# Optimization experiments

Hardware: AMD Instinct MI355X
Metric: run time of the kernel (lower is better)

## Reference

```python
import jax, jax.numpy as jnp
import numpy as np
import math

N = 60000          # nodes per node type
M = 60000          # edges per edge type
H = 64             # hidden_dim
PE = 4             # pe_dim
L = 3              # message passing layers
E = 24             # edge types
PE_LEN = 2 * N     # pe table length = 2 * num_pick_nodes
T = 6              # node types: object, ssBox, place_frame, ssCylinder, pick, place

# (src_type, dst_type) index per edge type, following detailed_edge_types order
SRC = np.array([0,1,2,1,2,0,4,5,0,1,2,3,0,4,2,4,3,4,0,5,3,5,2,5])
DST = np.array([1,0,1,2,0,2,5,4,0,1,2,3,4,0,4,2,4,3,5,0,5,3,5,2])


def posenc(n, d):
    pos = jnp.arange(n, dtype=jnp.float32)[:, None]
    div = jnp.exp(jnp.arange(0, d, 2, dtype=jnp.float32) * (-math.log(10000.0) / d))
    ang = pos * div  # [n, d//2]
    return jnp.stack([jnp.sin(ang), jnp.cos(ang)], axis=-1).reshape(n, d)


def setup_inputs():
    key = jax.random.key(0)
    ks = iter(jax.random.split(key, 48))
    def n_(shape, fan):
        return jax.random.normal(next(ks), shape, dtype=jnp.float32) / np.sqrt(fan).astype(np.float32)
    def ti(shape, hi):
        return jax.random.randint(next(ks), shape, 0, hi, dtype=jnp.int32)
    inp = {}
    inp['x_object'] = jax.random.normal(next(ks), (N, 4), dtype=jnp.float32)
    inp['x_ssBox'] = jax.random.normal(next(ks), (N, 4), dtype=jnp.float32)
    inp['x_place_frame'] = jax.random.normal(next(ks), (N, 4), dtype=jnp.float32)
    inp['x_ssCylinder'] = jax.random.normal(next(ks), (N, 3), dtype=jnp.float32)
    for nt in ['object', 'ssBox', 'place_frame', 'ssCylinder', 'pick', 'place']:
        inp['times_' + nt] = ti((N,), PE_LEN)
    inp['edge_index'] = ti((E, 2, M), N)
    inp['W_object'] = n_((8, H), 8); inp['b_object'] = jnp.zeros((H,), jnp.float32)
    inp['W_ssBox'] = n_((8, H), 8); inp['b_ssBox'] = jnp.zeros((H,), jnp.float32)
    inp['W_place_frame'] = n_((8, H), 8); inp['b_place_frame'] = jnp.zeros((H,), jnp.float32)
    inp['W_ssCylinder'] = n_((7, H), 7); inp['b_ssCylinder'] = jnp.zeros((H,), jnp.float32)
    inp['W_pick'] = n_((PE, H), PE); inp['b_pick'] = jnp.zeros((H,), jnp.float32)
    inp['W_place'] = n_((PE, H), PE); inp['b_place'] = jnp.zeros((H,), jnp.float32)
    inp['Wl'] = n_((L, E, H, H), H)
    inp['bl'] = jnp.zeros((L, E, H), jnp.float32)
    inp['Wr'] = n_((L, E, H, H), H)
    inp['Wm1'] = n_((H, H // 4), H); inp['bm1'] = jnp.zeros((H // 4,), jnp.float32)
    inp['Wm2'] = n_((H // 4, 1), H // 4); inp['bm2'] = jnp.zeros((1,), jnp.float32)
    return inp


def _forward(x_object, x_ssBox, x_place_frame, x_ssCylinder,
             W_object, b_object, W_ssBox, b_ssBox, W_place_frame, b_place_frame,
             W_ssCylinder, b_ssCylinder, W_pick, b_pick, W_place, b_place,
             Wl, bl, Wr, Wm1, bm1, Wm2, bm2,
             times_object, times_ssBox, times_place_frame, times_ssCylinder,
             times_pick, times_place, edge_index):
    pe = posenc(PE_LEN, PE)
    def emb(x, t, W, b):  # features || pe[times] -> linear
        return jnp.concatenate([x, pe[t]], axis=1) @ W + b
    X = jnp.stack([
        emb(x_object, times_object, W_object, b_object),
        emb(x_ssBox, times_ssBox, W_ssBox, b_ssBox),
        emb(x_place_frame, times_place_frame, W_place_frame, b_place_frame),
        emb(x_ssCylinder, times_ssCylinder, W_ssCylinder, b_ssCylinder),
        pe[times_pick] @ W_pick + b_pick,    # constraint nodes: pe -> linear
        pe[times_place] @ W_place + b_place,
    ])  # [T, N, H]

    src_e = edge_index[:, 0]  # [E, M]
    dst_e = edge_index[:, 1]  # [E, M]
    seg_sum = jax.vmap(lambda v, s: jax.ops.segment_sum(v, s, num_segments=N))
    counts = seg_sum(jnp.ones((E, M), jnp.float32), dst_e)  # [E, N] in-degree per edge type
    denom = jnp.maximum(counts, 1.0)[..., None]

    for l in range(L):
        # gather src node states per edge type: [E, M, H]
        msgs = jnp.take_along_axis(X[SRC], src_e[..., None], axis=1)
        # mean aggregation into dst nodes per edge type (SAGEConv aggr='mean')
        agg = seg_sum(msgs, dst_e) / denom  # [E, N, H]
        # out = lin_l(agg) + lin_r(x_dst) per edge type
        out_et = (jnp.einsum('enh,ehk->enk', agg, Wl[l]) + bl[l][:, None, :]
                  + jnp.einsum('enh,ehk->enk', X[DST], Wr[l]))  # [E, N, H]
        # sum contributions across edge types sharing a dst node type
        X = jax.ops.segment_sum(out_et, DST, num_segments=T)
        X = jax.nn.relu(X)

    # pool constraint (pick/place) node embeddings into a graph embedding
    graph_emb = X[4].sum(axis=0) + X[5].sum(axis=0)  # [H]
    h = jax.nn.relu(graph_emb)          # OutputMLP: act, (dropout=id), linear
    h = jax.nn.relu(h @ Wm1 + bm1)
    return h @ Wm2 + bm2                # [output_dim]


def reference(x_object, x_ssBox, x_place_frame, x_ssCylinder,
              times_object, times_ssBox, times_place_frame, times_ssCylinder,
              times_pick, times_place, edge_index,
              W_object, b_object, W_ssBox, b_ssBox, W_place_frame, b_place_frame,
              W_ssCylinder, b_ssCylinder, W_pick, b_pick, W_place, b_place,
              Wl, bl, Wr, Wm1, bm1, Wm2, bm2):
    return _forward(x_object, x_ssBox, x_place_frame, x_ssCylinder,
                    W_object, b_object, W_ssBox, b_ssBox, W_place_frame, b_place_frame,
                    W_ssCylinder, b_ssCylinder, W_pick, b_pick, W_place, b_place,
                    Wl, bl, Wr, Wm1, bm1, Wm2, bm2,
                    times_object, times_ssBox, times_place_frame, times_ssCylinder,
                    times_pick, times_place, edge_index)
```

## Files before the change

### kernel.cpp

```cpp
#include <hip/hip_runtime.h>


#define NN 60000
#define MM 60000
#define EE 24
#define TT 6
#define NTILES ((NN + 63) / 64)
#define SCH 2048
#define SNB ((NN + SCH - 1) / SCH)
#define CSRCAP 180

typedef unsigned short u16;
typedef unsigned int   u32;
typedef __attribute__((ext_vector_type(8))) short bf16x8;
typedef __attribute__((ext_vector_type(4))) float f32x4;

__constant__ int c_SRC[EE] = {0,1,2,1,2,0,4,5,0,1,2,3,0,4,2,4,3,4,0,5,3,5,2,5};
__constant__ int c_ELIST[TT][5] = {{1,4,8,13,19},{0,2,9,0,0},{3,5,10,15,23},
                                   {11,17,21,0,0},{7,12,14,16,0},{6,18,20,22,0}};
__constant__ int c_ECOUNT[TT] = {5,3,5,3,4,4};
__constant__ int c_TLIST[3][6] = {{0,1,2,3,4,5},{0,2,3,4,5,0},{4,5,0,0,0,0}};

__device__ __forceinline__ float lo16(u32 u){ union{u32 i; float f;} x; x.i = u << 16; return x.f; }
__device__ __forceinline__ float hi16(u32 u){ union{u32 i; float f;} x; x.i = u & 0xFFFF0000u; return x.f; }
__device__ __forceinline__ float bf2f(u16 u){ union{u32 i; float f;} x; x.i = (u32)u << 16; return x.f; }
__device__ __forceinline__ u16 f2bf(float f){
  union{float f; u32 i;} x; x.f = f;
  u32 r = (x.i + 0x7FFFu + ((x.i >> 16) & 1u)) >> 16;
  return (u16)r;
}
__device__ __forceinline__ u32 pack2(float a, float b){ return (u32)f2bf(a) | ((u32)f2bf(b) << 16); }

__global__ __launch_bounds__(256) void k_init(
    const float* __restrict__ Wl, const float* __restrict__ bl, const float* __restrict__ Wr,
    const int* __restrict__ tm0, const int* __restrict__ tm1,
    const int* __restrict__ tm2, const int* __restrict__ tm3,
    const int* __restrict__ tm4, const int* __restrict__ tm5,
    u16* __restrict__ WlT, u16* __restrict__ WrTs, float* __restrict__ blsum,
    float4* __restrict__ pe, int* __restrict__ counts, float* __restrict__ gemb)
{
  const int total1 = 3*EE*4096;
  const int total2 = 3*TT*4096;
  const int total3 = 3*TT*64;
  const int total4 = TT*NN;
  const int total5 = EE*NN;
  const int T12 = total1 + total2;
  const int T13 = T12 + total3;
  const int T14 = T13 + total4;
  const int T15 = T14 + total5;
  const int total = T15 + 64;
  for (int i = blockIdx.x*blockDim.x + threadIdx.x; i < total; i += gridDim.x*blockDim.x) {
    if (i < total1) {
      int h = i & 63, ko = (i >> 6) & 63, le = i >> 12;
      WlT[i] = f2bf(Wl[(size_t)le*4096 + h*64 + ko]);
    } else if (i < T12) {
      int j = i - total1;
      int h = j & 63, ko = (j >> 6) & 63, lt = j >> 12;
      int l = lt / TT, t = lt % TT;
      float s = 0.f;
      for (int q = 0; q < c_ECOUNT[t]; ++q) {
        int e = c_ELIST[t][q];
        s += Wr[((size_t)(l*EE + e)*64 + h)*64 + ko];
      }
      WrTs[j] = f2bf(s);
    } else if (i < T13) {
      int j = i - T12;
      int k = j & 63, lt = j >> 6;
      int l = lt / TT, t = lt % TT;
      float s = 0.f;
      for (int q = 0; q < c_ECOUNT[t]; ++q) s += bl[(size_t)(l*EE + c_ELIST[t][q])*64 + k];
      blsum[j] = s;
    } else if (i < T14) {
      int j = i - T13;
      int t = j / NN, n = j - t*NN;
      int tm;
      switch (t) {
        case 0:  tm = tm0[n]; break;
        case 1:  tm = tm1[n]; break;
        case 2:  tm = tm2[n]; break;
        case 3:  tm = tm3[n]; break;
        case 4:  tm = tm4[n]; break;
        default: tm = tm5[n]; break;
      }
      const float a0 = (float)tm, a1 = a0 * 0.01f;
      float4 v;
      v.x = sinf(a0); v.y = cosf(a0); v.z = sinf(a1); v.w = cosf(a1);
      pe[j] = v;
    } else if (i < T15) {
      counts[i - T14] = 0;
    } else {
      gemb[i - T15] = 0.f;
    }
  }
}

__global__ __launch_bounds__(256) void k_embed(
    const float* __restrict__ x0, const float* __restrict__ x1,
    const float* __restrict__ x2, const float* __restrict__ x3,
    const float4* __restrict__ pe,
    const float* __restrict__ W0, const float* __restrict__ b0,
    const float* __restrict__ W1, const float* __restrict__ b1,
    const float* __restrict__ W2, const float* __restrict__ b2,
    const float* __restrict__ W3, const float* __restrict__ b3,
    const float* __restrict__ W4, const float* __restrict__ b4,
    const float* __restrict__ W5, const float* __restrict__ b5,
    u16* __restrict__ X)
{
  const int tid = threadIdx.x;
  const int t = blockIdx.y;
  const int n = blockIdx.x * 4 + (tid >> 6);
  const int k = tid & 63;
  const float4 p = pe[(size_t)t*NN + n];
  const float p0 = p.x, p1 = p.y, p2 = p.z, p3 = p.w;
  float acc;
  if (t == 0) {
    const float* x = x0 + (size_t)n*4;
    acc = b0[k] + x[0]*W0[k] + x[1]*W0[64+k] + x[2]*W0[128+k] + x[3]*W0[192+k]
        + p0*W0[256+k] + p1*W0[320+k] + p2*W0[384+k] + p3*W0[448+k];
  } else if (t == 1) {
    const float* x = x1 + (size_t)n*4;
    acc = b1[k] + x[0]*W1[k] + x[1]*W1[64+k] + x[2]*W1[128+k] + x[3]*W1[192+k]
        + p0*W1[256+k] + p1*W1[320+k] + p2*W1[384+k] + p3*W1[448+k];
  } else if (t == 2) {
    const float* x = x2 + (size_t)n*4;
    acc = b2[k] + x[0]*W2[k] + x[1]*W2[64+k] + x[2]*W2[128+k] + x[3]*W2[192+k]
        + p0*W2[256+k] + p1*W2[320+k] + p2*W2[384+k] + p3*W2[448+k];
  } else if (t == 3) {
    const float* x = x3 + (size_t)n*3;
    acc = b3[k] + x[0]*W3[k] + x[1]*W3[64+k] + x[2]*W3[128+k]
        + p0*W3[192+k] + p1*W3[256+k] + p2*W3[320+k] + p3*W3[384+k];
  } else if (t == 4) {
    acc = b4[k] + p0*W4[k] + p1*W4[64+k] + p2*W4[128+k] + p3*W4[192+k];
  } else {
    acc = b5[k] + p0*W5[k] + p1*W5[64+k] + p2*W5[128+k] + p3*W5[192+k];
  }
  X[((size_t)t*NN + n)*64 + k] = f2bf(acc);
}

__global__ __launch_bounds__(256) void k_count(const int* __restrict__ ei, int* __restrict__ counts) {
  for (int i = blockIdx.x*blockDim.x + threadIdx.x; i < EE*MM; i += gridDim.x*blockDim.x) {
    int e = i / MM, m = i - e*MM;
    int d = ei[(size_t)e*2*MM + MM + m];
    atomicAdd(&counts[(size_t)e*NN + d], 1);
  }
}

__global__ __launch_bounds__(256) void k_scan1(const int* __restrict__ counts, int* __restrict__ ctot) {
  const int e = blockIdx.y, ch = blockIdx.x;
  const int tid = threadIdx.x, lane = tid & 63, wid = tid >> 6;
  __shared__ int ws[4];
  int s = 0;
  for (int i = tid; i < SCH; i += 256) {
    int n = ch*SCH + i;
    if (n < NN) s += counts[(size_t)e*NN + n];
  }
  #pragma unroll
  for (int d = 1; d < 64; d <<= 1) s += __shfl_xor(s, d);
  if (lane == 0) ws[wid] = s;
  __syncthreads();
  if (tid == 0) ctot[e*SNB + ch] = ws[0] + ws[1] + ws[2] + ws[3];
}

__global__ __launch_bounds__(64) void k_scan2(int* __restrict__ ctot) {
  const int e = blockIdx.x, lane = threadIdx.x;
  int v = (lane < SNB) ? ctot[e*SNB + lane] : 0;
  int s = v;
  #pragma unroll
  for (int d = 1; d < 64; d <<= 1) { int u = __shfl_up(s, d); if (lane >= d) s += u; }
  if (lane < SNB) ctot[e*SNB + lane] = s - v;
}

__global__ __launch_bounds__(256) void k_scan3(const int* __restrict__ counts, const int* __restrict__ ctot,
                                               int* __restrict__ offs) {
  const int e = blockIdx.y, ch = blockIdx.x;
  const int tid = threadIdx.x, lane = tid & 63, wid = tid >> 6;
  __shared__ int ws[4];
  __shared__ int cbase;
  if (tid == 0) cbase = ctot[e*SNB + ch];
  __syncthreads();
  for (int i0 = 0; i0 < SCH; i0 += 256) {
    const int n = ch*SCH + i0 + tid;
    const int c = (n < NN) ? counts[(size_t)e*NN + n] : 0;
    int s = c;
    #pragma unroll
    for (int d = 1; d < 64; d <<= 1) { int u = __shfl_up(s, d); if (lane >= d) s += u; }
    if (lane == 63) ws[wid] = s;
    __syncthreads();
    int wbase = 0;
    for (int q = 0; q < wid; ++q) wbase += ws[q];
    if (n < NN) offs[(size_t)e*(NN+1) + n] = cbase + wbase + s - c;
    __syncthreads();
    if (tid == 0) cbase += ws[0] + ws[1] + ws[2] + ws[3];
    __syncthreads();
  }
  if (ch == SNB-1 && tid == 0) offs[(size_t)e*(NN+1) + NN] = cbase;
}

__global__ __launch_bounds__(256) void k_place(const int* __restrict__ ei, const int* __restrict__ offs,
                                               int* __restrict__ counts, int* __restrict__ csr) {
  for (int i = blockIdx.x*blockDim.x + threadIdx.x; i < EE*MM; i += gridDim.x*blockDim.x) {
    int e = i / MM, m = i - e*MM;
    int s = ei[(size_t)e*2*MM + m];
    int d = ei[(size_t)e*2*MM + MM + m];
    int old = atomicSub(&counts[(size_t)e*NN + d], 1);
    csr[(size_t)e*MM + offs[(size_t)e*(NN+1) + d] + old - 1] = s;
  }
}

struct WB { int offs_w[65]; int csr_w[CSRCAP]; };

__device__ __forceinline__ void mm_tile(f32x4 acc[4], const u16* la, const u16* lb, int lane, int w)
{
  const int arow = w*16 + (lane & 15);
  const int kel  = (lane >> 4) * 8;
  #pragma unroll
  for (int kb = 0; kb < 2; ++kb) {
    bf16x8 a = *(const bf16x8*)&la[arow*72 + kb*32 + kel];
    #pragma unroll
    for (int nt = 0; nt < 4; ++nt) {
      bf16x8 b = *(const bf16x8*)&lb[(nt*16 + (lane & 15))*72 + kb*32 + kel];
      acc[nt] = __builtin_amdgcn_mfma_f32_16x16x32_bf16(a, b, acc[nt], 0, 0, 0);
    }
  }
}

__global__ __launch_bounds__(256) void k_layer(
    const u16* __restrict__ Xin, u16* __restrict__ Xout,
    const int* __restrict__ offs, const int* __restrict__ csr,
    const u16* __restrict__ WlT, const u16* __restrict__ WrTs,
    const float* __restrict__ blsum, float* __restrict__ gemb, int l)
{
  __shared__ __align__(16) u16 lds_a[64*72];
  __shared__ __align__(16) u16 lds_b[64*72];
  __shared__ WB wbuf[2];
  __shared__ int ph_beg[8], ph_cnt[8];

  const int tid  = threadIdx.x;
  const int tile = blockIdx.x % NTILES;
  const int t    = c_TLIST[l][blockIdx.x / NTILES];
  const int n0   = tile * 64;
  const int lane = tid & 63;
  const int w    = tid >> 6;
  const int ec   = c_ECOUNT[t];

  if (tid < ec) {
    const int e2 = c_ELIST[t][tid];
    int hi = n0 + 64; if (hi > NN) hi = NN;
    int b  = offs[(size_t)e2*(NN+1) + n0];
    int en = offs[(size_t)e2*(NN+1) + hi];
    ph_beg[tid+1] = b; ph_cnt[tid+1] = en - b;
  }
  __syncthreads();

  auto stage_win = [&](int qp) {
    if (qp > ec) return;
    const int e2 = c_ELIST[t][qp-1];
    WB* w2 = &wbuf[qp & 1];
    const int beg2 = ph_beg[qp], cnt2 = ph_cnt[qp];
    if (tid < 65) {
      int idx = n0 + tid; if (idx > NN) idx = NN;
      w2->offs_w[tid] = offs[(size_t)e2*(NN+1) + idx] - beg2;
    }
    const int lim = cnt2 < CSRCAP ? cnt2 : CSRCAP;
    for (int i = tid; i < lim; i += 256) w2->csr_w[i] = csr[(size_t)e2*MM + beg2 + i];
  };

  f32x4 acc[4];
  #pragma unroll
  for (int i = 0; i < 4; ++i) acc[i] = (f32x4){0.f,0.f,0.f,0.f};

  {
    stage_win(1);
    const int r = tid >> 2, h0 = (tid & 3) * 16;
    const int n = n0 + r;
    uint4 v0 = {0,0,0,0}, v1 = {0,0,0,0};
    if (n < NN) {
      const uint4* p = (const uint4*)(Xin + ((size_t)t*NN + n)*64 + h0);
      v0 = p[0]; v1 = p[1];
    }
    *(uint4*)&lds_a[r*72 + h0]     = v0;
    *(uint4*)&lds_a[r*72 + h0 + 8] = v1;
    const uint4* q = (const uint4*)(WrTs + (size_t)(l*TT + t)*4096 + r*64 + h0);
    uint4 w0 = q[0], w1 = q[1];
    *(uint4*)&lds_b[r*72 + h0]     = w0;
    *(uint4*)&lds_b[r*72 + h0 + 8] = w1;
  }
  __syncthreads();
  mm_tile(acc, lds_a, lds_b, lane, w);

  for (int qq = 1; qq <= ec; ++qq) {
    const int e = c_ELIST[t][qq-1];
    const int s = c_SRC[e];
    __syncthreads();
    stage_win(qq + 1);
    {
      const WB* wb = &wbuf[qq & 1];
      const int beg = ph_beg[qq], cnt = ph_cnt[qq];
      const int r = tid >> 2;
      const int h0 = (tid & 3) * 16;
      const int n = n0 + r;
      const u16* Xs = Xin + (size_t)s * NN * 64;
      float a[16];
      #pragma unroll
      for (int i = 0; i < 16; ++i) a[i] = 0.f;
      if (n < NN) {
        const int b  = wb->offs_w[r];
        const int en = wb->offs_w[r+1];
        if (cnt <= CSRCAP) {
          uint4 A0, A1, B0, B1;
          int j = b;
          if (j < en) {
            const u16* xp = Xs + (size_t)wb->csr_w[j]*64 + h0;
            A0 = *(const uint4*)xp; A1 = *(const uint4*)(xp + 8);
          }
          if (j + 1 < en) {
            const u16* xp = Xs + (size_t)wb->csr_w[j+1]*64 + h0;
            B0 = *(const uint4*)xp; B1 = *(const uint4*)(xp + 8);
          }
          while (j < en) {
            a[0]+=lo16(A0.x); a[1]+=hi16(A0.x); a[2]+=lo16(A0.y); a[3]+=hi16(A0.y);
            a[4]+=lo16(A0.z); a[5]+=hi16(A0.z); a[6]+=lo16(A0.w); a[7]+=hi16(A0.w);
            a[8]+=lo16(A1.x); a[9]+=hi16(A1.x); a[10]+=lo16(A1.y); a[11]+=hi16(A1.y);
            a[12]+=lo16(A1.z); a[13]+=hi16(A1.z); a[14]+=lo16(A1.w); a[15]+=hi16(A1.w);
            if (j + 2 < en) {
              const u16* xp = Xs + (size_t)wb->csr_w[j+2]*64 + h0;
              A0 = *(const uint4*)xp; A1 = *(const uint4*)(xp + 8);
            }
            if (j + 1 < en) {
              a[0]+=lo16(B0.x); a[1]+=hi16(B0.x); a[2]+=lo16(B0.y); a[3]+=hi16(B0.y);
              a[4]+=lo16(B0.z); a[5]+=hi16(B0.z); a[6]+=lo16(B0.w); a[7]+=hi16(B0.w);
              a[8]+=lo16(B1.x); a[9]+=hi16(B1.x); a[10]+=lo16(B1.y); a[11]+=hi16(B1.y);
              a[12]+=lo16(B1.z); a[13]+=hi16(B1.z); a[14]+=lo16(B1.w); a[15]+=hi16(B1.w);
              if (j + 3 < en) {
                const u16* xp = Xs + (size_t)wb->csr_w[j+3]*64 + h0;
                B0 = *(const uint4*)xp; B1 = *(const uint4*)(xp + 8);
              }
            }
            j += 2;
          }
        } else {
          for (int j = b; j < en; ++j) {
            int sn = csr[(size_t)e*MM + beg + j];
            const u16* xp = Xs + (size_t)sn*64 + h0;
            uint4 c0 = *(const uint4*)xp, c1 = *(const uint4*)(xp + 8);
            a[0]+=lo16(c0.x); a[1]+=hi16(c0.x); a[2]+=lo16(c0.y); a[3]+=hi16(c0.y);
            a[4]+=lo16(c0.z); a[5]+=hi16(c0.z); a[6]+=lo16(c0.w); a[7]+=hi16(c0.w);
            a[8]+=lo16(c1.x); a[9]+=hi16(c1.x); a[10]+=lo16(c1.y); a[11]+=hi16(c1.y);
            a[12]+=lo16(c1.z); a[13]+=hi16(c1.z); a[14]+=lo16(c1.w); a[15]+=hi16(c1.w);
          }
        }
        const int d = en - b;
        const float rd = 1.0f / (float)(d > 1 ? d : 1);
        #pragma unroll
        for (int i = 0; i < 16; ++i) a[i] *= rd;
      }
      uint4 s0, s1;
      s0.x = pack2(a[0],a[1]);   s0.y = pack2(a[2],a[3]);
      s0.z = pack2(a[4],a[5]);   s0.w = pack2(a[6],a[7]);
      s1.x = pack2(a[8],a[9]);   s1.y = pack2(a[10],a[11]);
      s1.z = pack2(a[12],a[13]); s1.w = pack2(a[14],a[15]);
      *(uint4*)&lds_a[r*72 + h0]     = s0;
      *(uint4*)&lds_a[r*72 + h0 + 8] = s1;
    }
    {
      const int r2 = tid >> 2, g0 = (tid & 3) * 16;
      const uint4* p = (const uint4*)(WlT + (size_t)(l*EE + e)*4096 + r2*64 + g0);
      uint4 w0 = p[0], w1 = p[1];
      *(uint4*)&lds_b[r2*72 + g0]     = w0;
      *(uint4*)&lds_b[r2*72 + g0 + 8] = w1;
    }
    __syncthreads();
    mm_tile(acc, lds_a, lds_b, lane, w);
  }

  __syncthreads();
  {
    const int col = lane & 15;
    const int rb  = w*16 + ((lane >> 4) << 2);
    #pragma unroll
    for (int nt = 0; nt < 4; ++nt) {
      const float blv = blsum[(size_t)(l*TT + t)*64 + nt*16 + col];
      #pragma unroll
      for (int j = 0; j < 4; ++j) {
        const float v = fmaxf(acc[nt][j] + blv, 0.f);
        const int rl = rb + j;
        lds_a[rl*72 + nt*16 + col] = ((n0 + rl) < NN) ? f2bf(v) : (u16)0;
      }
    }
  }
  __syncthreads();
  if (l < 2) {
    const int r = tid >> 2, h0 = (tid & 3) * 16;
    const int n = n0 + r;
    if (n < NN) {
      uint4 v0 = *(const uint4*)&lds_a[r*72 + h0];
      uint4 v1 = *(const uint4*)&lds_a[r*72 + h0 + 8];
      uint4* dst = (uint4*)(Xout + ((size_t)t*NN + n)*64 + h0);
      dst[0] = v0; dst[1] = v1;
    }
  } else if (tid < 64) {
    float sm = 0.f;
    for (int r = 0; r < 64; ++r) sm += bf2f(lds_a[r*72 + tid]);
    atomicAdd(&gemb[tid], sm);
  }
}

__global__ void k_head(const float* __restrict__ gemb, const float* __restrict__ Wm1,
                       const float* __restrict__ bm1, const float* __restrict__ Wm2,
                       const float* __restrict__ bm2, float* __restrict__ out)
{
  __shared__ float h[64];
  __shared__ float h2[16];
  const int tid = threadIdx.x;
  if (tid < 64) h[tid] = fmaxf(gemb[tid], 0.f);
  __syncthreads();
  if (tid < 16) {
    float a = bm1[tid];
    for (int i = 0; i < 64; ++i) a += h[i] * Wm1[i*16 + tid];
    h2[tid] = fmaxf(a, 0.f);
  }
  __syncthreads();
  if (tid == 0) {
    float a = bm2[0];
    for (int j = 0; j < 16; ++j) a += h2[j] * Wm2[j];
    out[0] = a;
  }
}

extern "C" void kernel_launch(void* const* d_in, const int* in_sizes, int n_in,
                              void* d_out, int out_size, void* d_ws, size_t ws_size,
                              hipStream_t stream) {
  char* ws = (char*)d_ws;
  size_t off = 0;
  auto take = [&](size_t bytes) -> char* {
    char* p = ws + off;
    off += (bytes + 255) & ~(size_t)255;
    return p;
  };
  u16*   XA     = (u16*)  take((size_t)6*NN*64*2);
  u16*   XB     = (u16*)  take((size_t)6*NN*64*2);
  u16*   WlT    = (u16*)  take((size_t)3*EE*4096*2);
  u16*   WrTs   = (u16*)  take((size_t)3*TT*4096*2);
  float* blsum  = (float*)take((size_t)3*TT*64*4);
  int*   counts = (int*)  take((size_t)EE*NN*4);
  int*   offs   = (int*)  take((size_t)EE*(NN+1)*4);
  int*   csr    = (int*)  take((size_t)EE*MM*4);
  int*   ctot   = (int*)  take((size_t)EE*SNB*4);
  float* petab  = (float*)take((size_t)TT*NN*16);
  float* gemb   = (float*)take(64*4);
  (void)ws_size; (void)in_sizes; (void)n_in; (void)out_size;

  const float* Wl = (const float*)d_in[23];
  const float* bl = (const float*)d_in[24];
  const float* Wr = (const float*)d_in[25];

  k_init<<<2048, 256, 0, stream>>>(
      Wl, bl, Wr,
      (const int*)d_in[4], (const int*)d_in[5], (const int*)d_in[6],
      (const int*)d_in[7], (const int*)d_in[8], (const int*)d_in[9],
      WlT, WrTs, blsum, (float4*)petab, counts, gemb);

  k_embed<<<dim3(NN/4, 6), 256, 0, stream>>>(
      (const float*)d_in[0], (const float*)d_in[1], (const float*)d_in[2], (const float*)d_in[3],
      (const float4*)petab,
      (const float*)d_in[11], (const float*)d_in[12],
      (const float*)d_in[13], (const float*)d_in[14],
      (const float*)d_in[15], (const float*)d_in[16],
      (const float*)d_in[17], (const float*)d_in[18],
      (const float*)d_in[19], (const float*)d_in[20],
      (const float*)d_in[21], (const float*)d_in[22],
      XA);

  const int* ei = (const int*)d_in[10];
  k_count<<<2048, 256, 0, stream>>>(ei, counts);
  k_scan1<<<dim3(SNB, EE), 256, 0, stream>>>(counts, ctot);
  k_scan2<<<EE, 64, 0, stream>>>(ctot);
  k_scan3<<<dim3(SNB, EE), 256, 0, stream>>>(counts, ctot, offs);
  k_place<<<2048, 256, 0, stream>>>(ei, offs, counts, csr);

  k_layer<<<NTILES*6, 256, 0, stream>>>(XA, XB, offs, csr, WlT, WrTs, blsum, gemb, 0);
  k_layer<<<NTILES*5, 256, 0, stream>>>(XB, XA, offs, csr, WlT, WrTs, blsum, gemb, 1);
  k_layer<<<NTILES*2, 256, 0, stream>>>(XA, XB, offs, csr, WlT, WrTs, blsum, gemb, 2);

  k_head<<<1, 64, 0, stream>>>(gemb, (const float*)d_in[26], (const float*)d_in[27],
                               (const float*)d_in[28], (const float*)d_in[29], (float*)d_out);
}
```

Measured before the change: 528.2 us.

## Merge embed/count kernels, collapse scan passes, fuse head into final layer

Embedding and the edge-count atomics now run in one launch, with extra blocks handling the counting. The three-pass scan becomes one kernel where each chunk recomputes its prefix base by summing all earlier counts. The output MLP head runs in the last block of the final layer, found by a global done counter. This removes four kernel launches and their serialization gaps, at the cost of redundant prefix reads in the scan (up to 30 chunks' worth per block) and a fence plus atomic per block in the layer kernel.

```diff
diff --git a/kernel.cpp b/kernel.cpp
--- a/kernel.cpp
+++ b/kernel.cpp
@@ -9,6 +9,7 @@
 #define SCH 2048
 #define SNB ((NN + SCH - 1) / SCH)
 #define CSRCAP 180
+#define EMB_BLKS (NN / 4 * 6)
 
 typedef unsigned short u16;
 typedef unsigned int   u32;
@@ -37,7 +38,8 @@
     const int* __restrict__ tm2, const int* __restrict__ tm3,
     const int* __restrict__ tm4, const int* __restrict__ tm5,
     u16* __restrict__ WlT, u16* __restrict__ WrTs, float* __restrict__ blsum,
-    float4* __restrict__ pe, int* __restrict__ counts, float* __restrict__ gemb)
+    float4* __restrict__ pe, int* __restrict__ counts, float* __restrict__ gemb,
+    int* __restrict__ donectr)
 {
   const int total1 = 3*EE*4096;
   const int total2 = 3*TT*4096;
@@ -48,7 +50,7 @@
   const int T13 = T12 + total3;
   const int T14 = T13 + total4;
   const int T15 = T14 + total5;
-  const int total = T15 + 64;
+  const int total = T15 + 64 + 1;
   for (int i = blockIdx.x*blockDim.x + threadIdx.x; i < total; i += gridDim.x*blockDim.x) {
     if (i < total1) {
       int h = i & 63, ko = (i >> 6) & 63, le = i >> 12;
@@ -88,13 +90,15 @@
       pe[j] = v;
     } else if (i < T15) {
       counts[i - T14] = 0;
+    } else if (i < T15 + 64) {
+      gemb[i - T15] = 0.f;
     } else {
-      gemb[i - T15] = 0.f;
-    }
-  }
-}
-
-__global__ __launch_bounds__(256) void k_embed(
+      donectr[0] = 0;
+    }
+  }
+}
+
+__global__ __launch_bounds__(256) void k_embed_count(
     const float* __restrict__ x0, const float* __restrict__ x1,
     const float* __restrict__ x2, const float* __restrict__ x3,
     const float4* __restrict__ pe,
@@ -104,80 +108,65 @@
     const float* __restrict__ W3, const float* __restrict__ b3,
     const float* __restrict__ W4, const float* __restrict__ b4,
     const float* __restrict__ W5, const float* __restrict__ b5,
-    u16* __restrict__ X)
+    u16* __restrict__ X,
+    const int* __restrict__ ei, int* __restrict__ counts)
 {
+  const int bx = blockIdx.x;
   const int tid = threadIdx.x;
-  const int t = blockIdx.y;
-  const int n = blockIdx.x * 4 + (tid >> 6);
-  const int k = tid & 63;
-  const float4 p = pe[(size_t)t*NN + n];
-  const float p0 = p.x, p1 = p.y, p2 = p.z, p3 = p.w;
-  float acc;
-  if (t == 0) {
-    const float* x = x0 + (size_t)n*4;
-    acc = b0[k] + x[0]*W0[k] + x[1]*W0[64+k] + x[2]*W0[128+k] + x[3]*W0[192+k]
-        + p0*W0[256+k] + p1*W0[320+k] + p2*W0[384+k] + p3*W0[448+k];
-  } else if (t == 1) {
-    const float* x = x1 + (size_t)n*4;
-    acc = b1[k] + x[0]*W1[k] + x[1]*W1[64+k] + x[2]*W1[128+k] + x[3]*W1[192+k]
-        + p0*W1[256+k] + p1*W1[320+k] + p2*W1[384+k] + p3*W1[448+k];
-  } else if (t == 2) {
-    const float* x = x2 + (size_t)n*4;
-    acc = b2[k] + x[0]*W2[k] + x[1]*W2[64+k] + x[2]*W2[128+k] + x[3]*W2[192+k]
-        + p0*W2[256+k] + p1*W2[320+k] + p2*W2[384+k] + p3*W2[448+k];
-  } else if (t == 3) {
-    const float* x = x3 + (size_t)n*3;
-    acc = b3[k] + x[0]*W3[k] + x[1]*W3[64+k] + x[2]*W3[128+k]
-        + p0*W3[192+k] + p1*W3[256+k] + p2*W3[320+k] + p3*W3[384+k];
-  } else if (t == 4) {
-    acc = b4[k] + p0*W4[k] + p1*W4[64+k] + p2*W4[128+k] + p3*W4[192+k];
+  if (bx < EMB_BLKS) {
+    const int t = bx / (NN/4);
+    const int n = (bx % (NN/4)) * 4 + (tid >> 6);
+    const int k = tid & 63;
+    const float4 p = pe[(size_t)t*NN + n];
+    const float p0 = p.x, p1 = p.y, p2 = p.z, p3 = p.w;
+    float acc;
+    if (t == 0) {
+      const float* x = x0 + (size_t)n*4;
+      acc = b0[k] + x[0]*W0[k] + x[1]*W0[64+k] + x[2]*W0[128+k] + x[3]*W0[192+k]
+          + p0*W0[256+k] + p1*W0[320+k] + p2*W0[384+k] + p3*W0[448+k];
+    } else if (t == 1) {
+      const float* x = x1 + (size_t)n*4;
+      acc = b1[k] + x[0]*W1[k] + x[1]*W1[64+k] + x[2]*W1[128+k] + x[3]*W1[192+k]
+          + p0*W1[256+k] + p1*W1[320+k] + p2*W1[384+k] + p3*W1[448+k];
+    } else if (t == 2) {
+      const float* x = x2 + (size_t)n*4;
+      acc = b2[k] + x[0]*W2[k] + x[1]*W2[64+k] + x[2]*W2[128+k] + x[3]*W2[192+k]
+          + p0*W2[256+k] + p1*W2[320+k] + p2*W2[384+k] + p3*W2[448+k];
+    } else if (t == 3) {
+      const float* x = x3 + (size_t)n*3;
+      acc = b3[k] + x[0]*W3[k] + x[1]*W3[64+k] + x[2]*W3[128+k]
+          + p0*W3[192+k] + p1*W3[256+k] + p2*W3[320+k] + p3*W3[384+k];
+    } else if (t == 4) {
+      acc = b4[k] + p0*W4[k] + p1*W4[64+k] + p2*W4[128+k] + p3*W4[192+k];
+    } else {
+      acc = b5[k] + p0*W5[k] + p1*W5[64+k] + p2*W5[128+k] + p3*W5[192+k];
+    }
+    X[((size_t)t*NN + n)*64 + k] = f2bf(acc);
   } else {
-    acc = b5[k] + p0*W5[k] + p1*W5[64+k] + p2*W5[128+k] + p3*W5[192+k];
-  }
-  X[((size_t)t*NN + n)*64 + k] = f2bf(acc);
-}
-
-__global__ __launch_bounds__(256) void k_count(const int* __restrict__ ei, int* __restrict__ counts) {
-  for (int i = blockIdx.x*blockDim.x + threadIdx.x; i < EE*MM; i += gridDim.x*blockDim.x) {
-    int e = i / MM, m = i - e*MM;
-    int d = ei[(size_t)e*2*MM + MM + m];
-    atomicAdd(&counts[(size_t)e*NN + d], 1);
-  }
-}
-
-__global__ __launch_bounds__(256) void k_scan1(const int* __restrict__ counts, int* __restrict__ ctot) {
-  const int e = blockIdx.y, ch = blockIdx.x;
-  const int tid = threadIdx.x, lane = tid & 63, wid = tid >> 6;
-  __shared__ int ws[4];
-  int s = 0;
-  for (int i = tid; i < SCH; i += 256) {
-    int n = ch*SCH + i;
-    if (n < NN) s += counts[(size_t)e*NN + n];
-  }
-  #pragma unroll
-  for (int d = 1; d < 64; d <<= 1) s += __shfl_xor(s, d);
-  if (lane == 0) ws[wid] = s;
-  __syncthreads();
-  if (tid == 0) ctot[e*SNB + ch] = ws[0] + ws[1] + ws[2] + ws[3];
-}
-
-__global__ __launch_bounds__(64) void k_scan2(int* __restrict__ ctot) {
-  const int e = blockIdx.x, lane = threadIdx.x;
-  int v = (lane < SNB) ? ctot[e*SNB + lane] : 0;
-  int s = v;
-  #pragma unroll
-  for (int d = 1; d < 64; d <<= 1) { int u = __shfl_up(s, d); if (lane >= d) s += u; }
-  if (lane < SNB) ctot[e*SNB + lane] = s - v;
-}
-
-__global__ __launch_bounds__(256) void k_scan3(const int* __restrict__ counts, const int* __restrict__ ctot,
-                                               int* __restrict__ offs) {
+    for (int i = (bx - EMB_BLKS)*256 + tid; i < EE*MM; i += 2048*256) {
+      int e = i / MM, m = i - e*MM;
+      int d = ei[(size_t)e*2*MM + MM + m];
+      atomicAdd(&counts[(size_t)e*NN + d], 1);
+    }
+  }
+}
+
+__global__ __launch_bounds__(256) void k_scan(const int* __restrict__ counts, int* __restrict__ offs) {
   const int e = blockIdx.y, ch = blockIdx.x;
   const int tid = threadIdx.x, lane = tid & 63, wid = tid >> 6;
   __shared__ int ws[4];
   __shared__ int cbase;
-  if (tid == 0) cbase = ctot[e*SNB + ch];
-  __syncthreads();
+  {
+    int s = 0;
+    const int lim = ch * SCH;
+    for (int i = tid; i < lim; i += 256) s += counts[(size_t)e*NN + i];
+    #pragma unroll
+    for (int d = 1; d < 64; d <<= 1) s += __shfl_xor(s, d);
+    if (lane == 0) ws[wid] = s;
+    __syncthreads();
+    if (tid == 0) cbase = ws[0] + ws[1] + ws[2] + ws[3];
+    __syncthreads();
+  }
   for (int i0 = 0; i0 < SCH; i0 += 256) {
     const int n = ch*SCH + i0 + tid;
     const int c = (n < NN) ? counts[(size_t)e*NN + n] : 0;
@@ -228,7 +217,10 @@
     const u16* __restrict__ Xin, u16* __restrict__ Xout,
     const int* __restrict__ offs, const int* __restrict__ csr,
     const u16* __restrict__ WlT, const u16* __restrict__ WrTs,
-    const float* __restrict__ blsum, float* __restrict__ gemb, int l)
+    const float* __restrict__ blsum, float* __restrict__ gemb, int l,
+    const float* __restrict__ Wm1, const float* __restrict__ bm1,
+    const float* __restrict__ Wm2, const float* __restrict__ bm2,
+    float* __restrict__ out, int* __restrict__ donectr)
 {
   __shared__ __align__(16) u16 lds_a[64*72];
   __shared__ __align__(16) u16 lds_b[64*72];
@@ -398,32 +390,34 @@
       uint4* dst = (uint4*)(Xout + ((size_t)t*NN + n)*64 + h0);
       dst[0] = v0; dst[1] = v1;
     }
-  } else if (tid < 64) {
-    float sm = 0.f;
-    for (int r = 0; r < 64; ++r) sm += bf2f(lds_a[r*72 + tid]);
-    atomicAdd(&gemb[tid], sm);
-  }
-}
-
-__global__ void k_head(const float* __restrict__ gemb, const float* __restrict__ Wm1,
-                       const float* __restrict__ bm1, const float* __restrict__ Wm2,
-                       const float* __restrict__ bm2, float* __restrict__ out)
-{
-  __shared__ float h[64];
-  __shared__ float h2[16];
-  const int tid = threadIdx.x;
-  if (tid < 64) h[tid] = fmaxf(gemb[tid], 0.f);
-  __syncthreads();
-  if (tid < 16) {
-    float a = bm1[tid];
-    for (int i = 0; i < 64; ++i) a += h[i] * Wm1[i*16 + tid];
-    h2[tid] = fmaxf(a, 0.f);
-  }
-  __syncthreads();
-  if (tid == 0) {
-    float a = bm2[0];
-    for (int j = 0; j < 16; ++j) a += h2[j] * Wm2[j];
-    out[0] = a;
+  } else {
+    if (tid < 64) {
+      float sm = 0.f;
+      for (int r = 0; r < 64; ++r) sm += bf2f(lds_a[r*72 + tid]);
+      atomicAdd(&gemb[tid], sm);
+    }
+    __threadfence();
+    __shared__ int amLast;
+    if (tid == 0) amLast = (atomicAdd(donectr, 1) == (int)gridDim.x - 1) ? 1 : 0;
+    __syncthreads();
+    if (amLast) {
+      __threadfence();
+      __shared__ float h[64];
+      __shared__ float h2[16];
+      if (tid < 64) h[tid] = fmaxf(atomicAdd(&gemb[tid], 0.f), 0.f);
+      __syncthreads();
+      if (tid < 16) {
+        float a = bm1[tid];
+        for (int i = 0; i < 64; ++i) a += h[i] * Wm1[i*16 + tid];
+        h2[tid] = fmaxf(a, 0.f);
+      }
+      __syncthreads();
+      if (tid == 0) {
+        float a = bm2[0];
+        for (int j = 0; j < 16; ++j) a += h2[j] * Wm2[j];
+        out[0] = a;
+      }
+    }
   }
 }
 
@@ -437,30 +431,35 @@
     off += (bytes + 255) & ~(size_t)255;
     return p;
   };
-  u16*   XA     = (u16*)  take((size_t)6*NN*64*2);
-  u16*   XB     = (u16*)  take((size_t)6*NN*64*2);
-  u16*   WlT    = (u16*)  take((size_t)3*EE*4096*2);
-  u16*   WrTs   = (u16*)  take((size_t)3*TT*4096*2);
-  float* blsum  = (float*)take((size_t)3*TT*64*4);
-  int*   counts = (int*)  take((size_t)EE*NN*4);
-  int*   offs   = (int*)  take((size_t)EE*(NN+1)*4);
-  int*   csr    = (int*)  take((size_t)EE*MM*4);
-  int*   ctot   = (int*)  take((size_t)EE*SNB*4);
-  float* petab  = (float*)take((size_t)TT*NN*16);
-  float* gemb   = (float*)take(64*4);
+  u16*   XA      = (u16*)  take((size_t)6*NN*64*2);
+  u16*   XB      = (u16*)  take((size_t)6*NN*64*2);
+  u16*   WlT     = (u16*)  take((size_t)3*EE*4096*2);
+  u16*   WrTs    = (u16*)  take((size_t)3*TT*4096*2);
+  float* blsum   = (float*)take((size_t)3*TT*64*4);
+  int*   counts  = (int*)  take((size_t)EE*NN*4);
+  int*   offs    = (int*)  take((size_t)EE*(NN+1)*4);
+  int*   csr     = (int*)  take((size_t)EE*MM*4);
+  float* petab   = (float*)take((size_t)TT*NN*16);
+  float* gemb    = (float*)take(64*4);
+  int*   donectr = (int*)  take(4);
   (void)ws_size; (void)in_sizes; (void)n_in; (void)out_size;
 
   const float* Wl = (const float*)d_in[23];
   const float* bl = (const float*)d_in[24];
   const float* Wr = (const float*)d_in[25];
+  const float* Wm1 = (const float*)d_in[26];
+  const float* bm1 = (const float*)d_in[27];
+  const float* Wm2 = (const float*)d_in[28];
+  const float* bm2 = (const float*)d_in[29];
 
   k_init<<<2048, 256, 0, stream>>>(
       Wl, bl, Wr,
       (const int*)d_in[4], (const int*)d_in[5], (const int*)d_in[6],
       (const int*)d_in[7], (const int*)d_in[8], (const int*)d_in[9],
-      WlT, WrTs, blsum, (float4*)petab, counts, gemb);
-
-  k_embed<<<dim3(NN/4, 6), 256, 0, stream>>>(
+      WlT, WrTs, blsum, (float4*)petab, counts, gemb, donectr);
+
+  const int* ei = (const int*)d_in[10];
+  k_embed_count<<<EMB_BLKS + 2048, 256, 0, stream>>>(
       (const float*)d_in[0], (const float*)d_in[1], (const float*)d_in[2], (const float*)d_in[3],
       (const float4*)petab,
       (const float*)d_in[11], (const float*)d_in[12],
@@ -469,19 +468,15 @@
       (const float*)d_in[17], (const float*)d_in[18],
       (const float*)d_in[19], (const float*)d_in[20],
       (const float*)d_in[21], (const float*)d_in[22],
-      XA);
-
-  const int* ei = (const int*)d_in[10];
-  k_count<<<2048, 256, 0, stream>>>(ei, counts);
-  k_scan1<<<dim3(SNB, EE), 256, 0, stream>>>(counts, ctot);
-  k_scan2<<<EE, 64, 0, stream>>>(ctot);
-  k_scan3<<<dim3(SNB, EE), 256, 0, stream>>>(counts, ctot, offs);
+      XA, ei, counts);
+
+  k_scan<<<dim3(SNB, EE), 256, 0, stream>>>(counts, offs);
   k_place<<<2048, 256, 0, stream>>>(ei, offs, counts, csr);
 
-  k_layer<<<NTILES*6, 256, 0, stream>>>(XA, XB, offs, csr, WlT, WrTs, blsum, gemb, 0);
-  k_layer<<<NTILES*5, 256, 0, stream>>>(XB, XA, offs, csr, WlT, WrTs, blsum, gemb, 1);
-  k_layer<<<NTILES*2, 256, 0, stream>>>(XA, XB, offs, csr, WlT, WrTs, blsum, gemb, 2);
-
-  k_head<<<1, 64, 0, stream>>>(gemb, (const float*)d_in[26], (const float*)d_in[27],
-                               (const float*)d_in[28], (const float*)d_in[29], (float*)d_out);
-}
+  k_layer<<<NTILES*6, 256, 0, stream>>>(XA, XB, offs, csr, WlT, WrTs, blsum, gemb, 0,
+                                        Wm1, bm1, Wm2, bm2, (float*)d_out, donectr);
+  k_layer<<<NTILES*5, 256, 0, stream>>>(XB, XA, offs, csr, WlT, WrTs, blsum, gemb, 1,
+                                        Wm1, bm1, Wm2, bm2, (float*)d_out, donectr);
+  k_layer<<<NTILES*2, 256, 0, stream>>>(XA, XB, offs, csr, WlT, WrTs, blsum, gemb, 2,
+                                        Wm1, bm1, Wm2, bm2, (float*)d_out, donectr);
+}
```

After: 715.3 us. +35.4%, slower.
